# Optimization experiments

Hardware: AMD Instinct MI355X
Metric: run time of the kernel (lower is better)

The kernel has to match this reference:

```python
import jax, jax.numpy as jnp
import numpy as np

B, N, DIM = 2, 4096, 512
HEADS, HEAD_DIM = 8, 64
INNER = HEADS * HEAD_DIM


def setup_inputs() -> dict:
    key = jax.random.key(0)
    k1, k2, k3 = jax.random.split(key, 3)
    x = jax.random.normal(k1, (B, N, DIM), dtype=jnp.float32)
    w_qkv = jax.random.normal(k2, (DIM, 3 * INNER), dtype=jnp.float32) * (DIM ** -0.5)
    temperature = jnp.asarray(np.log(HEAD_DIM ** -0.5), dtype=jnp.float32)
    w_out = jax.random.normal(k3, (INNER, DIM), dtype=jnp.float32) * (INNER ** -0.5)
    b_out = jnp.zeros((DIM,), dtype=jnp.float32)
    return {"x": x, "w_qkv": w_qkv, "temperature": temperature, "w_out": w_out, "b_out": b_out}


def reference(x, w_qkv, temperature, w_out, b_out):
    b, n, _ = x.shape
    qkv = x @ w_qkv                                   # (B, N, 3*inner)
    q, k, v = jnp.split(qkv, 3, axis=-1)
    # Faithful to original: raw reshape (NOT transpose) into (B, H, N, d)
    q = q.reshape(b, HEADS, n, HEAD_DIM)
    k = k.reshape(b, HEADS, n, HEAD_DIM)
    v = v.reshape(b, HEADS, n, HEAD_DIM)
    scores = jnp.einsum('bhnd,bhmd->bhnm', q, k) * jnp.exp(temperature)
    mask = jnp.eye(n, dtype=bool)                     # diagonal self-mask
    mask_value = jnp.finfo(scores.dtype).min
    scores = jnp.where(mask, mask_value, scores)
    attn = jax.nn.softmax(scores, axis=-1)
    out = jnp.einsum('bhnm,bhmd->bhnd', attn, v)      # (B, H, N, d)
    # Faithful to original: raw reshape (NOT transpose) back to (B, N, H*d)
    out = out.reshape(b, n, HEADS * HEAD_DIM)
    return out @ w_out + b_out                        # dropout inactive at inference
```

## Files before the change

kernel.cpp:

```cpp
#include <hip/hip_runtime.h>


typedef __bf16 bf16;
typedef __bf16 bf16x8 __attribute__((ext_vector_type(8)));
typedef __bf16 bf16x4 __attribute__((ext_vector_type(4)));
typedef float  f32x4  __attribute__((ext_vector_type(4)));

#define MFMA_BF16(a, b, c) __builtin_amdgcn_mfma_f32_16x16x32_bf16((a), (b), (c), 0, 0, 0)

__device__ __forceinline__ void gld_lds16(void* lds, const void* g) {
  __builtin_amdgcn_global_load_lds(
      (const __attribute__((address_space(1))) void*)g,
      (__attribute__((address_space(3))) void*)lds, 16, 0, 0);
}


__global__ void cast4_kernel(const float* __restrict__ in, bf16* __restrict__ out, int n4) {
  int i = blockIdx.x * 256 + threadIdx.x;
  if (i >= n4) return;
  float4 v = ((const float4*)in)[i];
  bf16x4 o;
  o[0] = (bf16)v.x; o[1] = (bf16)v.y; o[2] = (bf16)v.z; o[3] = (bf16)v.w;
  *(bf16x4*)(out + 4 * i) = o;
}

__global__ void wtrans_kernel(const float* __restrict__ in, bf16* __restrict__ out, int C) {
  __shared__ float tile[64 * 65];
  const int t = threadIdx.x;
  const int c0 = blockIdx.x * 64, r0 = blockIdx.y * 64;
#pragma unroll
  for (int p = 0; p < 16; p++) {
    int idx = p * 256 + t, r = idx >> 6, c = idx & 63;
    tile[r * 65 + c] = in[(r0 + r) * C + c0 + c];
  }
  __syncthreads();
#pragma unroll
  for (int p = 0; p < 16; p++) {
    int idx = p * 256 + t, c = idx >> 6, r = idx & 63;
    out[(size_t)(c0 + c) * 512 + r0 + r] = (bf16)tile[r * 65 + c];
  }
}

__global__ void vtrans_kernel(const bf16* __restrict__ V, bf16* __restrict__ Vt) {
  __shared__ bf16 tile[64 * 65];
  const int t = threadIdx.x;
  const size_t base = (size_t)blockIdx.y << 18;
  const int n0 = blockIdx.x * 64;
#pragma unroll
  for (int p = 0; p < 16; p++) {
    int idx = p * 256 + t, r = idx >> 6, c = idx & 63;
    tile[r * 65 + c] = V[base + (size_t)(n0 + r) * 64 + c];
  }
  __syncthreads();
#pragma unroll
  for (int p = 0; p < 16; p++) {
    int idx = p * 256 + t, d = idx >> 6, n = idx & 63;
    Vt[base + (size_t)d * 4096 + n0 + n] = tile[n * 65 + d];
  }
}


template<int EPI, int WNT>
__global__ __launch_bounds__(256) void gemm_bt(
    const bf16* __restrict__ A, const bf16* __restrict__ Bt,
    bf16* __restrict__ oQ, bf16* __restrict__ oK, bf16* __restrict__ oV,
    float* __restrict__ oC, const float* __restrict__ bias,
    const float* __restrict__ temp)
{
  __shared__ bf16 As[128 * 32];
  __shared__ bf16 Bs[WNT * 32 * 32];

  const int t    = threadIdx.x;
  const int lane = t & 63;
  const int w    = t >> 6;
  const int mm   = lane & 15;
  const int q    = lane >> 4;
  const int wm   = w >> 1, wn = w & 1;
  const int m0   = blockIdx.y * 128;
  const int n0   = blockIdx.x * (WNT * 32);

  const int srow = t >> 2, sch = t & 3;
  const int gch  = sch ^ ((srow >> 1) & 3);
  const bf16* Ab = A  + (m0 + srow) * 512 + gch * 8;
  const bf16* Bb = Bt + (n0 + srow) * 512 + gch * 8;
  bf16* Asl = As + t * 8;
  bf16* Bsl = Bs + t * 8;

  const int fslot = (q ^ ((mm >> 1) & 3)) * 8;

  const f32x4 zero4 = {0.f, 0.f, 0.f, 0.f};
  f32x4 acc[4][WNT];
#pragma unroll
  for (int i = 0; i < 4; i++)
#pragma unroll
    for (int j = 0; j < WNT; j++) acc[i][j] = zero4;

  for (int k0 = 0; k0 < 512; k0 += 32) {
    __syncthreads();
    gld_lds16(Asl,        Ab + k0);
    gld_lds16(Asl + 2048, Ab + 64 * 512 + k0);
    gld_lds16(Bsl,        Bb + k0);
    if (WNT == 4) gld_lds16(Bsl + 2048, Bb + 64 * 512 + k0);
    __syncthreads();

    bf16x8 af[4], bfv[WNT];
#pragma unroll
    for (int i = 0; i < 4; i++)
      af[i] = *(const bf16x8*)(As + (wm * 64 + i * 16 + mm) * 32 + fslot);
#pragma unroll
    for (int j = 0; j < WNT; j++)
      bfv[j] = *(const bf16x8*)(Bs + (wn * (WNT * 16) + j * 16 + mm) * 32 + fslot);

#pragma unroll
    for (int i = 0; i < 4; i++)
#pragma unroll
      for (int j = 0; j < WNT; j++)
        acc[i][j] = MFMA_BF16(af[i], bfv[j], acc[i][j]);
  }

  if (EPI == 0) {
    const float scale = __expf(temp[0]);
#pragma unroll
    for (int i = 0; i < 4; i++) {
      const int row = m0 + wm * 64 + i * 16 + q * 4;
#pragma unroll
      for (int j = 0; j < WNT; j++) {
        const int col = n0 + wn * (WNT * 16) + j * 16 + mm;
        bf16* dst; int c2; float s;
        if (col < 512)       { dst = oQ; c2 = col;        s = scale; }
        else if (col < 1024) { dst = oK; c2 = col - 512;  s = 1.0f;  }
        else                 { dst = oV; c2 = col - 1024; s = 1.0f;  }
#pragma unroll
        for (int r = 0; r < 4; r++)
          dst[(size_t)(row + r) * 512 + c2] = (bf16)(acc[i][j][r] * s);
      }
    }
  } else {
#pragma unroll
    for (int i = 0; i < 4; i++) {
      const int row = m0 + wm * 64 + i * 16 + q * 4;
#pragma unroll
      for (int j = 0; j < WNT; j++) {
        const int col = n0 + wn * (WNT * 16) + j * 16 + mm;
        const float b = bias[col];
#pragma unroll
        for (int r = 0; r < 4; r++)
          oC[(size_t)(row + r) * 512 + col] = acc[i][j][r] + b;
      }
    }
  }
}


template<int SPLIT>
__global__ __launch_bounds__(256, 4) void attn_kernel(
    const bf16* __restrict__ Q, const bf16* __restrict__ Kb,
    const bf16* __restrict__ Vt, bf16* __restrict__ O,
    float* __restrict__ Opart, float* __restrict__ Lpart)
{
  __shared__ bf16 Ks[64 * 64];
  __shared__ bf16 Vs[64 * 64];
  __shared__ bf16 Ps[4 * 32 * 72];

  const int t    = threadIdx.x;
  const int lane = t & 63;
  const int w    = t >> 6;
  const int mm   = lane & 15;
  const int q    = lane >> 4;
  const int bh   = blockIdx.y;
  const int q0   = blockIdx.x * 128;
  const int z    = blockIdx.z;
  const int KVLEN  = 4096 / SPLIT;
  const int kvbase = z * KVLEN;
  const size_t hb = (size_t)bh << 18;
  const bf16* Qh = Q  + hb;
  const bf16* Kh = Kb + hb;
  const bf16* Vh = Vt + hb;
  const int wrow = w * 32;

  bf16x8 qf[2][2];
#pragma unroll
  for (int i = 0; i < 2; i++)
#pragma unroll
    for (int ks = 0; ks < 2; ks++)
      qf[i][ks] = *(const bf16x8*)(Qh + (size_t)(q0 + wrow + i * 16 + mm) * 64 + ks * 32 + q * 8);

  const f32x4 zero4 = {0.f, 0.f, 0.f, 0.f};
  f32x4 o[2][4];
  float lsum[2] = {0.f, 0.f};
#pragma unroll
  for (int i = 0; i < 2; i++)
#pragma unroll
    for (int dj = 0; dj < 4; dj++) o[i][dj] = zero4;

  const int r0 = t >> 3, c0 = t & 7;
  const int g0 = c0 ^ (r0 & 7);
  bf16* Ksl = Ks + t * 8;
  bf16* Vsl = Vs + t * 8;
  bf16* pw  = Ps + w * (32 * 72);

  const int diagkv0 = (q0 + wrow) & ~63;

  for (int kv0 = kvbase; kv0 < kvbase + KVLEN; kv0 += 64) {
    __syncthreads();
    gld_lds16(Ksl,        Kh + (size_t)(kv0 + r0) * 64 + g0 * 8);
    gld_lds16(Ksl + 2048, Kh + (size_t)(kv0 + 32 + r0) * 64 + g0 * 8);
    gld_lds16(Vsl,        Vh + (size_t)r0 * 4096 + kv0 + g0 * 8);
    gld_lds16(Vsl + 2048, Vh + (size_t)(32 + r0) * 4096 + kv0 + g0 * 8);
    __syncthreads();

    f32x4 s[4][2];
#pragma unroll
    for (int jm = 0; jm < 4; jm++) {
      const int krow = jm * 16 + mm;
      const int sw = krow & 7;
      bf16x8 kf0 = *(const bf16x8*)(Ks + krow * 64 + ((q)     ^ sw) * 8);
      bf16x8 kf1 = *(const bf16x8*)(Ks + krow * 64 + ((4 + q) ^ sw) * 8);
#pragma unroll
      for (int i = 0; i < 2; i++) {
        f32x4 zacc = MFMA_BF16(kf0, qf[i][0], zero4);
        s[jm][i]   = MFMA_BF16(kf1, qf[i][1], zacc);
      }
    }

    if (kv0 == diagkv0) {
#pragma unroll
      for (int jm = 0; jm < 4; jm++)
#pragma unroll
        for (int i = 0; i < 2; i++)
#pragma unroll
          for (int r = 0; r < 4; r++) {
            const int rowg = q0 + wrow + i * 16 + mm;
            const int colg = kv0 + jm * 16 + q * 4 + r;
            if (rowg == colg) s[jm][i][r] = -1e30f;
          }
    }

#pragma unroll
    for (int i = 0; i < 2; i++) {
#pragma unroll
      for (int jm = 0; jm < 4; jm++) {
        bf16x4 pk;
        float ps = 0.f;
#pragma unroll
        for (int r = 0; r < 4; r++) {
          float p = __builtin_amdgcn_exp2f(
              __builtin_fmaf(s[jm][i][r], 1.44269504088896f, -17.3123404906676f));
          ps += p;
          pk[r] = (bf16)p;
        }
        lsum[i] += ps;
        *(bf16x4*)(pw + (i * 16 + mm) * 72 + jm * 16 + q * 4) = pk;
      }
    }
    __asm__ volatile("s_waitcnt lgkmcnt(0)" ::: "memory");

#pragma unroll
    for (int ks = 0; ks < 2; ks++) {
      bf16x8 vf[4];
#pragma unroll
      for (int dj = 0; dj < 4; dj++) {
        const int d = dj * 16 + mm;
        vf[dj] = *(const bf16x8*)(Vs + d * 64 + ((ks * 4 + q) ^ (d & 7)) * 8);
      }
#pragma unroll
      for (int i = 0; i < 2; i++) {
        bf16x8 pf = *(const bf16x8*)(pw + (i * 16 + mm) * 72 + ks * 32 + q * 8);
#pragma unroll
        for (int dj = 0; dj < 4; dj++)
          o[i][dj] = MFMA_BF16(pf, vf[dj], o[i][dj]);
      }
    }
  }

  float lred[2];
#pragma unroll
  for (int i = 0; i < 2; i++) {
    float v = lsum[i];
    v += __shfl_xor(v, 16);
    v += __shfl_xor(v, 32);
    lred[i] = v;
  }

  if (SPLIT == 2) {
    float* Op = Opart + ((size_t)z << 22) + hb;
    float* Lp = Lpart + (z << 16) + (bh << 12);
    if (q == 0) {
#pragma unroll
      for (int i = 0; i < 2; i++)
        Lp[q0 + wrow + i * 16 + mm] = lred[i];
    }
#pragma unroll
    for (int i = 0; i < 2; i++) {
      const int rowb = q0 + wrow + i * 16 + q * 4;
#pragma unroll
      for (int dj = 0; dj < 4; dj++)
#pragma unroll
        for (int r = 0; r < 4; r++)
          Op[(size_t)(rowb + r) * 64 + dj * 16 + mm] = o[i][dj][r];
    }
  } else {
    bf16* Oh = O + hb;
#pragma unroll
    for (int i = 0; i < 2; i++) {
      const int rowb = q0 + wrow + i * 16 + q * 4;
#pragma unroll
      for (int r = 0; r < 4; r++) {
        const float rinv = 1.0f / __shfl(lred[i], q * 4 + r);
#pragma unroll
        for (int dj = 0; dj < 4; dj++)
          Oh[(size_t)(rowb + r) * 64 + dj * 16 + mm] = (bf16)(o[i][dj][r] * rinv);
      }
    }
  }
}

__global__ void merge_kernel(const float* __restrict__ Op, const float* __restrict__ Lp,
                             bf16* __restrict__ Ob) {
  const int g = blockIdx.x * 256 + threadIdx.x;
  const int f = g * 4;
  const int row = f >> 6;
  const float rinv = 1.0f / (Lp[row] + Lp[(1 << 16) + row]);
  const float4 a = *(const float4*)(Op + f);
  const float4 b = *(const float4*)(Op + (1 << 22) + f);
  bf16x4 o;
  o[0] = (bf16)((a.x + b.x) * rinv);
  o[1] = (bf16)((a.y + b.y) * rinv);
  o[2] = (bf16)((a.z + b.z) * rinv);
  o[3] = (bf16)((a.w + b.w) * rinv);
  *(bf16x4*)(Ob + f) = o;
}


extern "C" void kernel_launch(void* const* d_in, const int* in_sizes, int n_in,
                              void* d_out, int out_size, void* d_ws, size_t ws_size,
                              hipStream_t stream) {
  const float* x      = (const float*)d_in[0];
  const float* w_qkv  = (const float*)d_in[1];
  const float* temp   = (const float*)d_in[2];
  const float* w_out  = (const float*)d_in[3];
  const float* b_out  = (const float*)d_in[4];
  float* out          = (float*)d_out;

  char* ws = (char*)d_ws;
  bf16*  Xb    = (bf16*)(ws);
  bf16*  Wt    = (bf16*)(ws + (size_t)(8u  << 20));
  bf16*  Qb    = (bf16*)(ws + (size_t)(10u << 20));
  bf16*  Kb    = (bf16*)(ws + (size_t)(18u << 20));
  bf16*  Vb    = (bf16*)(ws + (size_t)(26u << 20));
  bf16*  Vtb   = (bf16*)(ws + (size_t)(34u << 20));
  bf16*  Ob    = (bf16*)(ws + (size_t)(42u << 20));
  bf16*  Wot   = (bf16*)(ws + (size_t)(50u << 20));
  float* Lpart = (float*)(ws + (size_t)(51u << 20));
  float* Opart = (float*)(ws + (size_t)(52u << 20));

  const int split = (ws_size >= ((size_t)85u << 20)) ? 2 : 1;

  cast4_kernel<<<4096, 256, 0, stream>>>(x, Xb, (8192 * 512) / 4);
  wtrans_kernel<<<dim3(24, 8), 256, 0, stream>>>(w_qkv, Wt, 1536);
  wtrans_kernel<<<dim3(8, 8), 256, 0, stream>>>(w_out, Wot, 512);

  gemm_bt<0, 4><<<dim3(12, 64), 256, 0, stream>>>(Xb, Wt, Qb, Kb, Vb, nullptr, nullptr, temp);

  vtrans_kernel<<<dim3(64, 16), 256, 0, stream>>>(Vb, Vtb);

  if (split == 2) {
    attn_kernel<2><<<dim3(32, 16, 2), 256, 0, stream>>>(Qb, Kb, Vtb, nullptr, Opart, Lpart);
    merge_kernel<<<4096, 256, 0, stream>>>(Opart, Lpart, Ob);
  } else {
    attn_kernel<1><<<dim3(32, 16, 1), 256, 0, stream>>>(Qb, Kb, Vtb, Ob, nullptr, nullptr);
  }

  gemm_bt<1, 2><<<dim3(8, 64), 256, 0, stream>>>(Ob, Wot, nullptr, nullptr, nullptr, out, b_out, nullptr);
}
```

Before: 212.2 us.

## Enlarge attention Q tile, use MFMA row sums, fold log2e into Q, add split-3

Each attention block now handles 256 query rows, 64 per wave, so every K/V tile loaded into LDS is reused by twice as many queries. The log2(e) factor moves into the Q scale in the QKV GEMM epilogue, and the constant offset is dropped, so the exp no longer needs an FMA. Row sums are computed with an extra MFMA against a ones vector instead of scalar adds and shuffles. A three-way KV split with a templated merge is added when the workspace is large enough, which trades more partial-output traffic and lower occupancy (launch bounds 4→3, larger P buffer) for more parallel blocks.

Measured after the change: 207.5 us. 2.2% less time.

```diff
diff --git a/kernel.cpp b/kernel.cpp
--- a/kernel.cpp
+++ b/kernel.cpp
@@ -119,7 +119,7 @@
   }
 
   if (EPI == 0) {
-    const float scale = __expf(temp[0]);
+    const float scale = __expf(temp[0]) * 1.44269504088896f;
 #pragma unroll
     for (int i = 0; i < 4; i++) {
       const int row = m0 + wm * 64 + i * 16 + q * 4;
@@ -153,14 +153,14 @@
 
 
 template<int SPLIT>
-__global__ __launch_bounds__(256, 4) void attn_kernel(
+__global__ __launch_bounds__(256, 3) void attn_kernel(
     const bf16* __restrict__ Q, const bf16* __restrict__ Kb,
     const bf16* __restrict__ Vt, bf16* __restrict__ O,
     float* __restrict__ Opart, float* __restrict__ Lpart)
 {
   __shared__ bf16 Ks[64 * 64];
   __shared__ bf16 Vs[64 * 64];
-  __shared__ bf16 Ps[4 * 32 * 72];
+  __shared__ bf16 Ps[4 * 64 * 72];
 
   const int t    = threadIdx.x;
   const int lane = t & 63;
@@ -168,40 +168,48 @@
   const int mm   = lane & 15;
   const int q    = lane >> 4;
   const int bh   = blockIdx.y;
-  const int q0   = blockIdx.x * 128;
+  const int q0   = blockIdx.x * 256;
   const int z    = blockIdx.z;
-  const int KVLEN  = 4096 / SPLIT;
-  const int kvbase = z * KVLEN;
   const size_t hb = (size_t)bh << 18;
   const bf16* Qh = Q  + hb;
   const bf16* Kh = Kb + hb;
   const bf16* Vh = Vt + hb;
-  const int wrow = w * 32;
-
-  bf16x8 qf[2][2];
-#pragma unroll
-  for (int i = 0; i < 2; i++)
+  const int q0w  = q0 + w * 64;
+
+  int tlo, tn;
+  if (SPLIT == 1)      { tlo = 0;                               tn = 64; }
+  else if (SPLIT == 2) { tlo = z * 32;                          tn = 32; }
+  else                 { tlo = (z == 0) ? 0 : (z == 1 ? 22 : 43); tn = (z == 0) ? 22 : 21; }
+
+  bf16x8 qf[4][2];
+#pragma unroll
+  for (int i = 0; i < 4; i++)
 #pragma unroll
     for (int ks = 0; ks < 2; ks++)
-      qf[i][ks] = *(const bf16x8*)(Qh + (size_t)(q0 + wrow + i * 16 + mm) * 64 + ks * 32 + q * 8);
+      qf[i][ks] = *(const bf16x8*)(Qh + (size_t)(q0w + i * 16 + mm) * 64 + ks * 32 + q * 8);
 
   const f32x4 zero4 = {0.f, 0.f, 0.f, 0.f};
-  f32x4 o[2][4];
-  float lsum[2] = {0.f, 0.f};
-#pragma unroll
-  for (int i = 0; i < 2; i++)
+  f32x4 o[4][4];
+  f32x4 lacc[4];
+#pragma unroll
+  for (int i = 0; i < 4; i++) {
+    lacc[i] = zero4;
 #pragma unroll
     for (int dj = 0; dj < 4; dj++) o[i][dj] = zero4;
+  }
+
+  bf16x8 onesf;
+#pragma unroll
+  for (int e = 0; e < 8; e++) onesf[e] = (bf16)1.0f;
 
   const int r0 = t >> 3, c0 = t & 7;
   const int g0 = c0 ^ (r0 & 7);
   bf16* Ksl = Ks + t * 8;
   bf16* Vsl = Vs + t * 8;
-  bf16* pw  = Ps + w * (32 * 72);
-
-  const int diagkv0 = (q0 + wrow) & ~63;
-
-  for (int kv0 = kvbase; kv0 < kvbase + KVLEN; kv0 += 64) {
+  bf16* pw  = Ps + w * (64 * 72);
+
+  for (int it = 0; it < tn; it++) {
+    const int kv0 = (tlo + it) * 64;
     __syncthreads();
     gld_lds16(Ksl,        Kh + (size_t)(kv0 + r0) * 64 + g0 * 8);
     gld_lds16(Ksl + 2048, Kh + (size_t)(kv0 + 32 + r0) * 64 + g0 * 8);
@@ -209,7 +217,8 @@
     gld_lds16(Vsl + 2048, Vh + (size_t)(32 + r0) * 4096 + kv0 + g0 * 8);
     __syncthreads();
 
-    f32x4 s[4][2];
+    const bool diag = (kv0 == q0w);
+
 #pragma unroll
     for (int jm = 0; jm < 4; jm++) {
       const int krow = jm * 16 + mm;
@@ -217,39 +226,14 @@
       bf16x8 kf0 = *(const bf16x8*)(Ks + krow * 64 + ((q)     ^ sw) * 8);
       bf16x8 kf1 = *(const bf16x8*)(Ks + krow * 64 + ((4 + q) ^ sw) * 8);
 #pragma unroll
-      for (int i = 0; i < 2; i++) {
+      for (int i = 0; i < 4; i++) {
         f32x4 zacc = MFMA_BF16(kf0, qf[i][0], zero4);
-        s[jm][i]   = MFMA_BF16(kf1, qf[i][1], zacc);
-      }
-    }
-
-    if (kv0 == diagkv0) {
-#pragma unroll
-      for (int jm = 0; jm < 4; jm++)
-#pragma unroll
-        for (int i = 0; i < 2; i++)
-#pragma unroll
-          for (int r = 0; r < 4; r++) {
-            const int rowg = q0 + wrow + i * 16 + mm;
-            const int colg = kv0 + jm * 16 + q * 4 + r;
-            if (rowg == colg) s[jm][i][r] = -1e30f;
-          }
-    }
-
-#pragma unroll
-    for (int i = 0; i < 2; i++) {
-#pragma unroll
-      for (int jm = 0; jm < 4; jm++) {
+        f32x4 sv   = MFMA_BF16(kf1, qf[i][1], zacc);
+        if (diag && jm == i && (mm >> 2) == q) sv[mm & 3] = -1e30f;
         bf16x4 pk;
-        float ps = 0.f;
-#pragma unroll
-        for (int r = 0; r < 4; r++) {
-          float p = __builtin_amdgcn_exp2f(
-              __builtin_fmaf(s[jm][i][r], 1.44269504088896f, -17.3123404906676f));
-          ps += p;
-          pk[r] = (bf16)p;
-        }
-        lsum[i] += ps;
+#pragma unroll
+        for (int r = 0; r < 4; r++)
+          pk[r] = (bf16)__builtin_amdgcn_exp2f(sv[r]);
         *(bf16x4*)(pw + (i * 16 + mm) * 72 + jm * 16 + q * 4) = pk;
       }
     }
@@ -264,70 +248,68 @@
         vf[dj] = *(const bf16x8*)(Vs + d * 64 + ((ks * 4 + q) ^ (d & 7)) * 8);
       }
 #pragma unroll
-      for (int i = 0; i < 2; i++) {
+      for (int i = 0; i < 4; i++) {
         bf16x8 pf = *(const bf16x8*)(pw + (i * 16 + mm) * 72 + ks * 32 + q * 8);
 #pragma unroll
         for (int dj = 0; dj < 4; dj++)
           o[i][dj] = MFMA_BF16(pf, vf[dj], o[i][dj]);
-      }
-    }
-  }
-
-  float lred[2];
-#pragma unroll
-  for (int i = 0; i < 2; i++) {
-    float v = lsum[i];
-    v += __shfl_xor(v, 16);
-    v += __shfl_xor(v, 32);
-    lred[i] = v;
-  }
-
-  if (SPLIT == 2) {
+        lacc[i] = MFMA_BF16(pf, onesf, lacc[i]);
+      }
+    }
+  }
+
+  if (SPLIT == 1) {
+    bf16* Oh = O + hb;
+#pragma unroll
+    for (int i = 0; i < 4; i++) {
+      const int rowb = q0w + i * 16 + q * 4;
+#pragma unroll
+      for (int r = 0; r < 4; r++) {
+        const float rinv = 1.0f / lacc[i][r];
+#pragma unroll
+        for (int dj = 0; dj < 4; dj++)
+          Oh[(size_t)(rowb + r) * 64 + dj * 16 + mm] = (bf16)(o[i][dj][r] * rinv);
+      }
+    }
+  } else {
     float* Op = Opart + ((size_t)z << 22) + hb;
     float* Lp = Lpart + (z << 16) + (bh << 12);
-    if (q == 0) {
-#pragma unroll
-      for (int i = 0; i < 2; i++)
-        Lp[q0 + wrow + i * 16 + mm] = lred[i];
-    }
-#pragma unroll
-    for (int i = 0; i < 2; i++) {
-      const int rowb = q0 + wrow + i * 16 + q * 4;
+#pragma unroll
+    for (int i = 0; i < 4; i++) {
+      const int rowb = q0w + i * 16 + q * 4;
+      if (mm == 0) {
+#pragma unroll
+        for (int r = 0; r < 4; r++) Lp[rowb + r] = lacc[i][r];
+      }
 #pragma unroll
       for (int dj = 0; dj < 4; dj++)
 #pragma unroll
         for (int r = 0; r < 4; r++)
           Op[(size_t)(rowb + r) * 64 + dj * 16 + mm] = o[i][dj][r];
     }
-  } else {
-    bf16* Oh = O + hb;
-#pragma unroll
-    for (int i = 0; i < 2; i++) {
-      const int rowb = q0 + wrow + i * 16 + q * 4;
-#pragma unroll
-      for (int r = 0; r < 4; r++) {
-        const float rinv = 1.0f / __shfl(lred[i], q * 4 + r);
-#pragma unroll
-        for (int dj = 0; dj < 4; dj++)
-          Oh[(size_t)(rowb + r) * 64 + dj * 16 + mm] = (bf16)(o[i][dj][r] * rinv);
-      }
-    }
-  }
-}
-
+  }
+}
+
+template<int SPLIT>
 __global__ void merge_kernel(const float* __restrict__ Op, const float* __restrict__ Lp,
                              bf16* __restrict__ Ob) {
   const int g = blockIdx.x * 256 + threadIdx.x;
   const int f = g * 4;
   const int row = f >> 6;
-  const float rinv = 1.0f / (Lp[row] + Lp[(1 << 16) + row]);
-  const float4 a = *(const float4*)(Op + f);
-  const float4 b = *(const float4*)(Op + (1 << 22) + f);
+  float l = 0.f;
+  float4 a = {0.f, 0.f, 0.f, 0.f};
+#pragma unroll
+  for (int zz = 0; zz < SPLIT; zz++) {
+    l += Lp[(zz << 16) + row];
+    const float4 b = *(const float4*)(Op + ((size_t)zz << 22) + f);
+    a.x += b.x; a.y += b.y; a.z += b.z; a.w += b.w;
+  }
+  const float rinv = 1.0f / l;
   bf16x4 o;
-  o[0] = (bf16)((a.x + b.x) * rinv);
-  o[1] = (bf16)((a.y + b.y) * rinv);
-  o[2] = (bf16)((a.z + b.z) * rinv);
-  o[3] = (bf16)((a.w + b.w) * rinv);
+  o[0] = (bf16)(a.x * rinv);
+  o[1] = (bf16)(a.y * rinv);
+  o[2] = (bf16)(a.z * rinv);
+  o[3] = (bf16)(a.w * rinv);
   *(bf16x4*)(Ob + f) = o;
 }
 
@@ -354,7 +336,8 @@
   float* Lpart = (float*)(ws + (size_t)(51u << 20));
   float* Opart = (float*)(ws + (size_t)(52u << 20));
 
-  const int split = (ws_size >= ((size_t)85u << 20)) ? 2 : 1;
+  const int split = (ws_size >= ((size_t)103u << 20)) ? 3
+                  : (ws_size >= ((size_t)86u  << 20)) ? 2 : 1;
 
   cast4_kernel<<<4096, 256, 0, stream>>>(x, Xb, (8192 * 512) / 4);
   wtrans_kernel<<<dim3(24, 8), 256, 0, stream>>>(w_qkv, Wt, 1536);
@@ -364,11 +347,14 @@
 
   vtrans_kernel<<<dim3(64, 16), 256, 0, stream>>>(Vb, Vtb);
 
-  if (split == 2) {
-    attn_kernel<2><<<dim3(32, 16, 2), 256, 0, stream>>>(Qb, Kb, Vtb, nullptr, Opart, Lpart);
-    merge_kernel<<<4096, 256, 0, stream>>>(Opart, Lpart, Ob);
+  if (split == 3) {
+    attn_kernel<3><<<dim3(16, 16, 3), 256, 0, stream>>>(Qb, Kb, Vtb, nullptr, Opart, Lpart);
+    merge_kernel<3><<<4096, 256, 0, stream>>>(Opart, Lpart, Ob);
+  } else if (split == 2) {
+    attn_kernel<2><<<dim3(16, 16, 2), 256, 0, stream>>>(Qb, Kb, Vtb, nullptr, Opart, Lpart);
+    merge_kernel<2><<<4096, 256, 0, stream>>>(Opart, Lpart, Ob);
   } else {
-    attn_kernel<1><<<dim3(32, 16, 1), 256, 0, stream>>>(Qb, Kb, Vtb, Ob, nullptr, nullptr);
+    attn_kernel<1><<<dim3(16, 16, 1), 256, 0, stream>>>(Qb, Kb, Vtb, Ob, nullptr, nullptr);
   }
 
   gemm_bt<1, 2><<<dim3(8, 64), 256, 0, stream>>>(Ob, Wot, nullptr, nullptr, nullptr, out, b_out, nullptr);
```
